# Kernel optimization log

Hardware: AMD Instinct MI355X
Metric: run time of the kernel (lower is better)

## Reference

```python
import jax, jax.numpy as jnp
import numpy as np

NUM_FEATURE = 512
HIDDEN = 256
NUM_CLASSES = 10
L1 = 1e-4
ALPHA = 1e-3
BATCH = 65536


def setup_inputs() -> dict:
    key = jax.random.key(0)
    k = jax.random.split(key, 6)
    x = jax.random.normal(k[0], (BATCH, NUM_FEATURE), dtype=jnp.float32)
    y = jax.random.randint(k[1], (BATCH,), 0, NUM_CLASSES, dtype=jnp.int32)
    fc0 = jax.random.normal(k[2], (NUM_FEATURE, 512), dtype=jnp.float32) / NUM_FEATURE
    fc1 = jax.random.normal(k[3], (NUM_FEATURE, 512), dtype=jnp.float32) / NUM_FEATURE
    w = jax.random.normal(k[4], (NUM_FEATURE, HIDDEN), dtype=jnp.float32) / NUM_FEATURE
    w1 = jax.random.normal(k[5], (HIDDEN, NUM_CLASSES), dtype=jnp.float32) / HIDDEN
    return {"x": x, "y": y, "fc0": fc0, "fc1": fc1, "w": w, "w1": w1}


def reference(x, y, fc0, fc1, w, w1):
    # sigmoid-gated MLP block with residual
    x1 = x @ fc0                                   # [B, 512]
    x2 = jax.nn.relu(x @ fc1)                      # [B, 512]
    x4 = x + (1.0 + jax.nn.sigmoid(x1)) * x2       # [B, 512] residual

    # head (Dropout(p=0.0) is identity)
    logits = jax.nn.relu(x4 @ w) @ w1              # [B, 10]
    pred = jnp.argmax(logits, axis=1)

    # cross-entropy (mean over batch)
    logp = jax.nn.log_softmax(logits, axis=-1)
    ce = -jnp.mean(jnp.take_along_axis(logp, y[:, None].astype(jnp.int32), axis=1))

    # L1 penalty on all weight matrices
    l1_pen = L1 * (jnp.abs(w1).sum() + jnp.abs(w).sum()
                   + jnp.abs(fc0).sum() + jnp.abs(fc1).sum())

    # per-class variance: sum_i ||mean_{y_i} - x4_i||^2, vectorized via segment sums
    counts = jax.ops.segment_sum(jnp.ones((x4.shape[0],), jnp.float32), y,
                                 num_segments=NUM_CLASSES)
    sums = jax.ops.segment_sum(x4, y, num_segments=NUM_CLASSES)   # [10, 512]
    means = sums / jnp.maximum(counts, 1.0)[:, None]
    var_loss = jnp.sum(jnp.square(means[y] - x4))

    loss = ce + l1_pen + ALPHA * var_loss
    acc = jnp.mean((pred.astype(jnp.int32) == y.astype(jnp.int32)).astype(jnp.float32))
    return (loss, acc)
```

## Files before the change

### kernel.cpp

```cpp
#include <hip/hip_runtime.h>
#include <stdint.h>

#define BATCH 65536
#define FDIM 512
#define HDIM 256
#define NC 10
#define NREP 16

typedef short short8 __attribute__((ext_vector_type(8)));
typedef float f32x4 __attribute__((ext_vector_type(4)));

#define OFF_FC0T   ((size_t)0)
#define OFF_FC1T   (OFF_FC0T + (size_t)512*512*2)
#define OFF_WT     (OFF_FC1T + (size_t)512*512*2)
#define OFF_XT     (OFF_WT   + (size_t)256*512*2)
#define OFF_X4T    (OFF_XT   + (size_t)BATCH*512*2)
#define OFF_ACC    (OFF_X4T  + (size_t)BATCH*512*2)
#define SCAL_SUMSQ 0
#define SCAL_CE    16
#define SCAL_ACC   32
#define SCAL_L1    48
#define SCAL_N     128
#define CNT_OFF    SCAL_N
#define GSUM_OFF   (SCAL_N + NREP*16)
#define ACC_FLOATS (GSUM_OFF + NREP*5120)
#define OFF_W1T    (OFF_ACC + (size_t)ACC_FLOATS*4)

#define GLL(g,l) __builtin_amdgcn_global_load_lds((const __attribute__((address_space(1))) void*)(g), (__attribute__((address_space(3))) void*)(l), 16, 0, 0)

__device__ __forceinline__ unsigned short f2b(float f){
  unsigned u = __float_as_uint(f);
  u += 0x7FFFu + ((u >> 16) & 1u);
  return (unsigned short)(u >> 16);
}
__device__ __forceinline__ float b2f(unsigned short h){
  return __uint_as_float(((unsigned)h) << 16);
}
__device__ __forceinline__ unsigned pk2b(float f0, float f1){
  unsigned u0 = __float_as_uint(f0) + 0x8000u;
  unsigned u1 = __float_as_uint(f1) + 0x8000u;
  return __builtin_amdgcn_perm(u1, u0, 0x07060302u);
}

__global__ __launch_bounds__(256) void k_setup(
    const float* __restrict__ x,   const float* __restrict__ fc0,
    const float* __restrict__ fc1, const float* __restrict__ w,
    const float* __restrict__ w1,  const int* __restrict__ y,
    unsigned short* __restrict__ xT,   unsigned short* __restrict__ fc0T,
    unsigned short* __restrict__ fc1T, unsigned short* __restrict__ wT,
    unsigned short* __restrict__ w1T,  float* __restrict__ accb)
{
  int blk = blockIdx.x, t = threadIdx.x;
  if (blk < 1024){
    int I = blk*4 + (t >> 6);
    int l = t & 63;
    int row = I*16 + (l & 15), q = l >> 4;
    const float* src = x + (size_t)row*FDIM + q*8;
    #pragma unroll
    for (int C = 0; C < 16; ++C){
      float4 v0 = *(const float4*)(src + C*32);
      float4 v1 = *(const float4*)(src + C*32 + 4);
      unsigned o[4];
      o[0] = pk2b(v0.x, v0.y); o[1] = pk2b(v0.z, v0.w);
      o[2] = pk2b(v1.x, v1.y); o[3] = pk2b(v1.z, v1.w);
      *(short8*)&xT[(((size_t)I*16 + C) << 9) + l*8] = *(short8*)o;
    }
    return;
  }
  if (blk < 1360){
    int i = (blk - 1024)*256 + t;
    float l1v = 0.f;
    if (i < 32768){
      int n4 = i&15, m = (i>>4)&3, C = (i>>6)&15, J = i>>10;
      int n = J*16+n4, k8 = C*4+m;
      unsigned short o[8];
      #pragma unroll
      for (int j=0;j<8;++j){ float v = fc0[(size_t)(k8*8+j)*512 + n]; o[j]=f2b(v); l1v += fabsf(v); }
      *(short8*)&fc0T[(size_t)(J*16+C)*512 + (i&63)*8] = *(short8*)o;
    } else if (i < 65536){
      int j0 = i - 32768;
      int n4 = j0&15, m = (j0>>4)&3, C = (j0>>6)&15, J = j0>>10;
      int n = J*16+n4, k8 = C*4+m;
      unsigned short o[8];
      #pragma unroll
      for (int j=0;j<8;++j){ float v = fc1[(size_t)(k8*8+j)*512 + n]; o[j]=f2b(v); l1v += fabsf(v); }
      *(short8*)&fc1T[(size_t)(J*16+C)*512 + (j0&63)*8] = *(short8*)o;
    } else if (i < 81920){
      int j0 = i - 65536;
      int n4 = j0&15, m = (j0>>4)&3, C = (j0>>6)&15, J = j0>>10;
      int n = J*16+n4, k8 = C*4+m;
      unsigned short o[8];
      #pragma unroll
      for (int j=0;j<8;++j){ float v = w[(size_t)(k8*8+j)*256 + n]; o[j]=f2b(v); l1v += fabsf(v); }
      *(short8*)&wT[(size_t)(J*16+C)*512 + (j0&63)*8] = *(short8*)o;
    } else if (i < 86016){
      int j0 = i - 81920;
      int C = j0 >> 9, l = (j0 >> 3) & 63, e = j0 & 7;
      int n = l & 15, k = C*32 + (l>>4)*8 + e;
      float v = (n < NC) ? w1[k*NC + n] : 0.f;
      w1T[C*512 + l*8 + e] = f2b(v);
      if (n < NC) l1v = fabsf(v);
    }
    for (int off = 32; off; off >>= 1) l1v += __shfl_down(l1v, off);
    if ((t & 63) == 0 && l1v != 0.f)
      atomicAdd(&accb[SCAL_L1 + (blk & (NREP-1))], l1v);
    return;
  }
  if (blk < 1441){
    int base = (blk - 1360)*1024;
    #pragma unroll
    for (int j=0;j<4;++j){
      int idx = base + j*256 + t;
      if (idx < ACC_FLOATS && (idx < CNT_OFF || idx >= CNT_OFF + NREP*16))
        accb[idx] = 0.f;
    }
    return;
  }
  {
    __shared__ float cntS[16];
    int b = blk - 1441;
    if (t < 16) cntS[t] = 0.f;
    __syncthreads();
    int base = b*4096;
    for (int i = t; i < 4096; i += 256) atomicAdd(&cntS[y[base+i]], 1.f);
    __syncthreads();
    if (t < 16) accb[CNT_OFF + b*16 + t] = cntS[t];
  }
}


#define BARRIER() __builtin_amdgcn_s_barrier()
#define LGKM0() do{ asm volatile("s_waitcnt lgkmcnt(0)" ::: "memory"); \
                    __builtin_amdgcn_sched_barrier(0); }while(0)

#define READA(A, AB, H) do{                                                   \
  _Pragma("unroll") for (int c_=0;c_<2;++c_)                                  \
  _Pragma("unroll") for (int m_=0;m_<4;++m_)                                  \
    A[c_][m_] = *(const short8*)((AB) + (((wr*8 + (H)*4 + m_)*2 + c_)<<10) + lane*16); \
}while(0)

#define READB(B, BB, MAT) do{                                                 \
  _Pragma("unroll") for (int c_=0;c_<2;++c_)                                  \
  _Pragma("unroll") for (int n_=0;n_<2;++n_)                                  \
    B[c_][n_] = *(const short8*)((BB) + (MAT)*16384 + (((wc*2+n_)*2 + c_)<<10) + lane*16); \
}while(0)

#define MMALL(MB) do{                                                         \
  __builtin_amdgcn_s_setprio(1);                                              \
  _Pragma("unroll") for (int c_=0;c_<2;++c_)                                  \
  _Pragma("unroll") for (int n_=0;n_<2;++n_)                                  \
  _Pragma("unroll") for (int m_=0;m_<4;++m_)                                  \
    acc1[(MB)+m_][n_] = __builtin_amdgcn_mfma_f32_16x16x32_bf16(a[c_][m_], b0[c_][n_], acc1[(MB)+m_][n_], 0,0,0); \
  _Pragma("unroll") for (int c_=0;c_<2;++c_)                                  \
  _Pragma("unroll") for (int n_=0;n_<2;++n_)                                  \
  _Pragma("unroll") for (int m_=0;m_<4;++m_)                                  \
    acc2[(MB)+m_][n_] = __builtin_amdgcn_mfma_f32_16x16x32_bf16(a[c_][m_], b1[c_][n_], acc2[(MB)+m_][n_], 0,0,0); \
  __builtin_amdgcn_s_setprio(0);                                              \
}while(0)

#define STAGEA(KT2, H) do{                                                    \
  char* d_ = ldsd + (((KT2)&1) ? 65536 : 0);                                  \
  _Pragma("unroll") for (int r_=0;r_<2;++r_){                                 \
    int idx_ = r_*8 + wv, q_ = idx_>>1, C_ = idx_&1;                          \
    int Il_ = (q_&3) + ((q_>>2)<<3) + (H)*4;                                  \
    GLL(xb + (((size_t)((rowblk*16 + Il_)*16 + (KT2)*2 + C_)) << 10) + lane*16, \
        d_ + ((Il_*2 + C_) << 10) + lane*16);                                 \
  } }while(0)

#define STAGEB(KT2, MAT) do{                                                  \
  char* d_ = ldsd + (((KT2)&1) ? 65536 : 0) + 32768 + (MAT)*16384;            \
  const char* s_ = (MAT) ? b1b : b0b;                                         \
  _Pragma("unroll") for (int r_=0;r_<2;++r_){                                 \
    int idx_ = r_*8 + wv, J_ = idx_>>1, C_ = idx_&1;                          \
    GLL(s_ + (((size_t)((colblk*8 + J_)*16 + (KT2)*2 + C_)) << 10) + lane*16, \
        d_ + ((J_*2 + C_) << 10) + lane*16);                                  \
  } }while(0)

#define KLOOP_PROLOGUE() do{                                                  \
  STAGEA(0,0); STAGEA(0,1); STAGEB(0,0); STAGEB(0,1);                         \
  STAGEA(1,0); STAGEB(1,0);                                                   \
  asm volatile("s_waitcnt vmcnt(4)" ::: "memory");                            \
  __builtin_amdgcn_sched_barrier(0);                                          \
  BARRIER();                                                                  \
}while(0)

#define KLOOP_BODY(kt) do{                                                    \
  char* Ab = ldsd + (((kt)&1) ? 65536 : 0);                                   \
  char* Bb = Ab + 32768;                                                      \
                                                                      \
  READA(a, Ab, 0);                                                            \
  READB(b0, Bb, 0);                                                           \
  READB(b1, Bb, 1);                                                           \
  if ((kt) < 7){ STAGEA((kt)+1, 1); STAGEB((kt)+1, 1); }                      \
  BARRIER(); LGKM0();                                                         \
  MMALL(0);                                                                   \
  BARRIER();                                                                  \
                                                                      \
  READA(a, Ab, 1);                                                            \
  if ((kt) < 6){ STAGEA((kt)+2, 0); STAGEB((kt)+2, 0); }                      \
  BARRIER(); LGKM0();                                                         \
  MMALL(4);                                                                   \
  if ((kt) < 6)       { asm volatile("s_waitcnt vmcnt(4)" ::: "memory"); }    \
  else if ((kt) == 6) { asm volatile("s_waitcnt vmcnt(0)" ::: "memory"); }    \
  __builtin_amdgcn_sched_barrier(0);                                          \
  BARRIER();                                                                  \
}while(0)

__global__ __launch_bounds__(512, 2) void k_gemm12(
    const unsigned short* __restrict__ xT,
    const unsigned short* __restrict__ fc0T,
    const unsigned short* __restrict__ fc1T,
    unsigned short* __restrict__ x4T,
    float* __restrict__ scal)
{
  extern __shared__ __align__(16) char ldsd[];

  int blk = blockIdx.x;
  int wg = (blk & 7)*128 + (blk >> 3);
  int rowblk = wg >> 2;
  int colblk = wg & 3;

  int t = threadIdx.x;
  int wv = t >> 6, lane = t & 63, ln = lane & 15, quad = lane >> 4;
  int wr = wv >> 2, wc = wv & 3;

  const char* xb  = (const char*)xT;
  const char* b0b = (const char*)fc0T;
  const char* b1b = (const char*)fc1T;

  const f32x4 zv = {0.f,0.f,0.f,0.f};
  f32x4 acc1[8][2], acc2[8][2];
  #pragma unroll
  for (int m=0;m<8;++m){ acc1[m][0]=zv; acc1[m][1]=zv; acc2[m][0]=zv; acc2[m][1]=zv; }

  short8 a[2][4], b0[2][2], b1[2][2];

  KLOOP_PROLOGUE();
  for (int kt = 0; kt < 8; ++kt) KLOOP_BODY(kt);

  {
    int Cres = colblk*4 + wc;
    #pragma unroll
    for (int i = 0; i < 8; ++i){
      GLL(xb + (((size_t)((rowblk*16 + wr*8 + i)*16 + Cres)) << 10) + lane*16,
          ldsd + ((wv*8 + i) << 10) + lane*16);
    }
    asm volatile("s_waitcnt vmcnt(0)" ::: "memory");
  }
  __syncthreads();

  unsigned short* resU = (unsigned short*)ldsd;
  unsigned short* x4U  = (unsigned short*)(ldsd + 65536);
  float sumsq = 0.f;
  #pragma unroll
  for (int m = 0; m < 8; ++m){
    #pragma unroll
    for (int n = 0; n < 2; ++n){
      #pragma unroll
      for (int r = 0; r < 4; ++r){
        int slot = (quad*4 + r) | ((n*2 + (ln>>3)) << 4);
        int idx = ((wv*8 + m) << 9) + slot*8 + (ln & 7);
        float xv  = b2f(resU[idx]);
        float x1v = acc1[m][n][r];
        float x2v = fmaxf(acc2[m][n][r], 0.f);
        float gate = 1.f + 1.f/(1.f + __expf(-x1v));
        float x4v = fmaf(gate, x2v, xv);
        unsigned short ub = f2b(x4v);
        float fq = b2f(ub);
        sumsq = fmaf(fq, fq, sumsq);
        x4U[idx] = ub;
      }
    }
  }
  for (int off = 32; off; off >>= 1) sumsq += __shfl_down(sumsq, off);
  __syncthreads();
  float* red = (float*)ldsd;
  if (lane == 0) red[wv] = sumsq;
  __syncthreads();
  if (t == 0){
    float s = 0.f;
    #pragma unroll
    for (int i=0;i<8;++i) s += red[i];
    atomicAdd(&scal[SCAL_SUMSQ + (blk & (NREP-1))], s);
  }
  #pragma unroll
  for (int r = 0; r < 2; ++r){
    int o = r*512 + t;
    int tile = o >> 6, off16 = o & 63;
    int wvp = tile >> 3, i = tile & 7;
    size_t Ig = (size_t)rowblk*16 + (wvp>>2)*8 + i;
    int Cg = colblk*4 + (wvp & 3);
    *(short8*)&x4T[((Ig*16 + Cg) << 9) + off16*8] =
      *(const short8*)&x4U[(tile << 9) + off16*8];
  }
}

__global__ __launch_bounds__(256) void k_csum(const unsigned short* __restrict__ x4T,
                                              const int* __restrict__ y,
                                              float* __restrict__ gsum){
  int w = blockIdx.x*4 + (threadIdx.x >> 6);
  int l = threadIdx.x & 63;
  int C = w & 15, Ig = w >> 4;
  int rl = l & 15, q = l >> 4;
  float a[NC][8];
  #pragma unroll
  for (int c=0;c<NC;++c)
    #pragma unroll
    for (int e=0;e<8;++e) a[c][e]=0.f;
  for (int ii = 0; ii < 64; ++ii){
    int I = Ig*64 + ii;
    int yv = y[I*16 + rl];
    short8 v = *(const short8*)&x4T[(((size_t)I*16 + C) << 9) + l*8];
    float f[8];
    #pragma unroll
    for (int e=0;e<8;++e) f[e] = b2f((unsigned short)v[e]);
    #pragma unroll
    for (int c=0;c<NC;++c){
      bool m = (yv == c);
      #pragma unroll
      for (int e=0;e<8;++e) a[c][e] += m ? f[e] : 0.f;
    }
  }
  #pragma unroll
  for (int off = 1; off < 16; off <<= 1)
    #pragma unroll
    for (int c=0;c<NC;++c)
      #pragma unroll
      for (int e=0;e<8;++e) a[c][e] += __shfl_xor(a[c][e], off);
  if (rl == 0){
    int rep = Ig & (NREP-1);
    int kb = C*32 + q*8;
    #pragma unroll
    for (int c=0;c<NC;++c)
      #pragma unroll
      for (int e=0;e<8;++e)
        atomicAdd(&gsum[(size_t)rep*5120 + c*512 + kb + e], a[c][e]);
  }
}

__global__ __launch_bounds__(512, 2) void k_gemm3_head(
    const unsigned short* __restrict__ x4T,
    const unsigned short* __restrict__ wT,
    const unsigned short* __restrict__ w1T,
    const int* __restrict__ y,
    float* __restrict__ scal)
{
  extern __shared__ __align__(16) char ldsd[];
  __shared__ float redc[8], reda[8];

  int blk = blockIdx.x;
  int rowblk = blk;
  const int colblk = 0;

  int t = threadIdx.x;
  int wv = t >> 6, lane = t & 63, ln = lane & 15, quad = lane >> 4;
  int wr = wv >> 2, wc = wv & 3;
  int rep = (blk ^ (blk >> 4)) & (NREP-1);

  const char* xb  = (const char*)x4T;
  const char* b0b = (const char*)wT;
  const char* b1b = (const char*)wT + (size_t)128*1024;

  const f32x4 zv = {0.f,0.f,0.f,0.f};
  f32x4 acc1[8][2], acc2[8][2];
  #pragma unroll
  for (int m=0;m<8;++m){ acc1[m][0]=zv; acc1[m][1]=zv; acc2[m][0]=zv; acc2[m][1]=zv; }

  short8 a[2][4], b0[2][2], b1[2][2];

  KLOOP_PROLOGUE();
  for (int kt = 0; kt < 8; ++kt) KLOOP_BODY(kt);

  short8 bw1[8];
  #pragma unroll
  for (int Ck = 0; Ck < 8; ++Ck)
    bw1[Ck] = *(const short8*)&w1T[Ck*512 + lane*8];

  unsigned short* transH = (unsigned short*)ldsd;
  #pragma unroll
  for (int m = 0; m < 8; ++m){
    #pragma unroll
    for (int n = 0; n < 2; ++n){
      #pragma unroll
      for (int r = 0; r < 4; ++r){
        int slot = (quad*4 + r) | ((n*2 + (ln>>3)) << 4);
        int e = ln & 7;
        int IhA = wr*8 + m;
        transH[((IhA*8 + wc)     << 9) + slot*8 + e] = f2b(fmaxf(acc1[m][n][r], 0.f));
        transH[((IhA*8 + 4 + wc) << 9) + slot*8 + e] = f2b(fmaxf(acc2[m][n][r], 0.f));
      }
    }
  }
  __syncthreads();

  f32x4 alog[2] = {zv, zv};
  #pragma unroll
  for (int ih = 0; ih < 2; ++ih){
    int Ih = wv*2 + ih;
    #pragma unroll
    for (int Ck = 0; Ck < 8; ++Ck){
      short8 af = *(const short8*)&transH[((Ih*8 + Ck) << 9) + lane*8];
      alog[ih] = __builtin_amdgcn_mfma_f32_16x16x32_bf16(af, bw1[Ck], alog[ih], 0,0,0);
    }
  }

  float ce_l = 0.f, acc_l = 0.f;
  #pragma unroll
  for (int ih = 0; ih < 2; ++ih){
    #pragma unroll
    for (int r = 0; r < 4; ++r){
      int grow = blk*256 + (wv*2 + ih)*16 + quad*4 + r;
      int yv = y[grow];
      float lg = (ln < NC) ? alog[ih][r] : -1e30f;
      float m = lg; int mi = ln;
      #pragma unroll
      for (int mk = 1; mk < 16; mk <<= 1){
        float om = __shfl_xor(m, mk); int oi = __shfl_xor(mi, mk);
        if (om > m || (om == m && oi < mi)){ m = om; mi = oi; }
      }
      float e  = (ln < NC) ? __expf(lg - m) : 0.f;
      float sy = (ln == yv) ? lg : 0.f;
      #pragma unroll
      for (int mk = 1; mk < 16; mk <<= 1){ e += __shfl_xor(e, mk); sy += __shfl_xor(sy, mk); }
      float lse = m + __logf(e);
      if (ln == 0){ ce_l += (lse - sy); acc_l += (mi == yv) ? 1.f : 0.f; }
    }
  }
  ce_l  += __shfl_down(ce_l, 16);  acc_l += __shfl_down(acc_l, 16);
  ce_l  += __shfl_down(ce_l, 32);  acc_l += __shfl_down(acc_l, 32);
  if (lane == 0){ redc[wv] = ce_l; reda[wv] = acc_l; }
  __syncthreads();
  if (t == 0){
    float c = 0.f, aa = 0.f;
    #pragma unroll
    for (int i=0;i<8;++i){ c += redc[i]; aa += reda[i]; }
    atomicAdd(&scal[SCAL_CE  + rep], c);
    atomicAdd(&scal[SCAL_ACC + rep], aa);
  }
}

__global__ __launch_bounds__(1024) void k_final(const float* __restrict__ accb,
                                                float* __restrict__ out){
  const float* gsum = accb + GSUM_OFF;
  const float* gcnt = accb + CNT_OFF;
  int t = threadIdx.x;
  float contrib = 0.f;
  for (int idx = t; idx < 5120; idx += 1024){
    float S = 0.f;
    #pragma unroll
    for (int r = 0; r < NREP; ++r) S += gsum[(size_t)r*5120 + idx];
    int c = idx >> 9;
    float cnt = 0.f;
    #pragma unroll
    for (int r = 0; r < NREP; ++r) cnt += gcnt[r*16 + c];
    contrib += S*S / fmaxf(cnt, 1.f);
  }
  for (int off = 32; off; off >>= 1) contrib += __shfl_down(contrib, off);
  __shared__ float red[16];
  if ((t & 63) == 0) red[t >> 6] = contrib;
  __syncthreads();
  if (t == 0){
    float var2 = 0.f;
    #pragma unroll
    for (int i=0;i<16;++i) var2 += red[i];
    float sumsq=0.f, ce=0.f, acc=0.f, l1=0.f;
    for (int r=0;r<NREP;++r){
      sumsq += accb[SCAL_SUMSQ+r];
      ce    += accb[SCAL_CE+r];
      acc   += accb[SCAL_ACC+r];
      l1    += accb[SCAL_L1+r];
    }
    float var_loss = sumsq - var2;
    out[0] = ce/(float)BATCH + 1e-4f*l1 + 1e-3f*var_loss;
    out[1] = acc/(float)BATCH;
  }
}

extern "C" void kernel_launch(void* const* d_in, const int* in_sizes, int n_in,
                              void* d_out, int out_size, void* d_ws, size_t ws_size,
                              hipStream_t stream){
  (void)in_sizes; (void)n_in; (void)out_size; (void)ws_size;
  const float* x   = (const float*)d_in[0];
  const int*   y   = (const int*)d_in[1];
  const float* fc0 = (const float*)d_in[2];
  const float* fc1 = (const float*)d_in[3];
  const float* w   = (const float*)d_in[4];
  const float* w1  = (const float*)d_in[5];
  char* ws = (char*)d_ws;
  unsigned short* fc0T = (unsigned short*)(ws + OFF_FC0T);
  unsigned short* fc1T = (unsigned short*)(ws + OFF_FC1T);
  unsigned short* wT   = (unsigned short*)(ws + OFF_WT);
  unsigned short* xT   = (unsigned short*)(ws + OFF_XT);
  unsigned short* x4T  = (unsigned short*)(ws + OFF_X4T);
  unsigned short* w1T  = (unsigned short*)(ws + OFF_W1T);
  float* accb = (float*)(ws + OFF_ACC);
  float* scal = accb;
  float* gsum = accb + GSUM_OFF;

  static bool once = [](){
    hipFuncSetAttribute((const void*)k_gemm12,
                        hipFuncAttributeMaxDynamicSharedMemorySize, 131072);
    hipFuncSetAttribute((const void*)k_gemm3_head,
                        hipFuncAttributeMaxDynamicSharedMemorySize, 131072);
    return true;
  }();
  (void)once;

  k_setup<<<1457, 256, 0, stream>>>(x, fc0, fc1, w, w1, y, xT, fc0T, fc1T, wT, w1T, accb);
  k_gemm12<<<1024, 512, 131072, stream>>>(xT, fc0T, fc1T, x4T, scal);
  k_csum<<<256, 256, 0, stream>>>(x4T, y, gsum);
  k_gemm3_head<<<256, 512, 131072, stream>>>(x4T, wT, w1T, y, scal);
  k_final<<<1, 1024, 0, stream>>>(accb, (float*)d_out);
}
```

Baseline: 399.3 us.

## Restructure GEMM k-loop into finer stages with per-K-chunk register fragments

Replaces the two-phase k-loop body with an eight-phase schedule per pair of k-tiles. Each phase loads one K-chunk of A (all 8 row fragments) and a single B fragment pair, then runs 16 MFMAs on acc1 or acc2. Global-to-LDS staging is split into smaller per-chunk pieces interleaved across the phases. The aim is to cut register pressure for the A/B fragments and spread memory traffic more evenly against MFMA work. The cost is more barriers and waits per k-tile, plus reloading A fragments for each chunk.

```diff
diff --git a/kernel.cpp b/kernel.cpp
--- a/kernel.cpp
+++ b/kernel.cpp
@@ -133,77 +133,98 @@
 #define LGKM0() do{ asm volatile("s_waitcnt lgkmcnt(0)" ::: "memory"); \
                     __builtin_amdgcn_sched_barrier(0); }while(0)
 
-#define READA(A, AB, H) do{                                                   \
-  _Pragma("unroll") for (int c_=0;c_<2;++c_)                                  \
-  _Pragma("unroll") for (int m_=0;m_<4;++m_)                                  \
-    A[c_][m_] = *(const short8*)((AB) + (((wr*8 + (H)*4 + m_)*2 + c_)<<10) + lane*16); \
+#define RA(AB, C) do{                                                         \
+  _Pragma("unroll") for (int m_=0;m_<8;++m_)                                  \
+    a[m_] = *(const short8*)((AB) + (((wr*8+m_)*2 + (C))<<10) + lane*16);     \
 }while(0)
 
-#define READB(B, BB, MAT) do{                                                 \
-  _Pragma("unroll") for (int c_=0;c_<2;++c_)                                  \
+#define RB(AB, MAT, C) do{                                                    \
   _Pragma("unroll") for (int n_=0;n_<2;++n_)                                  \
-    B[c_][n_] = *(const short8*)((BB) + (MAT)*16384 + (((wc*2+n_)*2 + c_)<<10) + lane*16); \
+    bb[n_] = *(const short8*)((AB) + 32768 + (MAT)*16384 +                    \
+                              (((wc*2+n_)*2 + (C))<<10) + lane*16);           \
 }while(0)
 
-#define MMALL(MB) do{                                                         \
+#define MM16(ACC) do{                                                         \
   __builtin_amdgcn_s_setprio(1);                                              \
-  _Pragma("unroll") for (int c_=0;c_<2;++c_)                                  \
   _Pragma("unroll") for (int n_=0;n_<2;++n_)                                  \
-  _Pragma("unroll") for (int m_=0;m_<4;++m_)                                  \
-    acc1[(MB)+m_][n_] = __builtin_amdgcn_mfma_f32_16x16x32_bf16(a[c_][m_], b0[c_][n_], acc1[(MB)+m_][n_], 0,0,0); \
-  _Pragma("unroll") for (int c_=0;c_<2;++c_)                                  \
-  _Pragma("unroll") for (int n_=0;n_<2;++n_)                                  \
-  _Pragma("unroll") for (int m_=0;m_<4;++m_)                                  \
-    acc2[(MB)+m_][n_] = __builtin_amdgcn_mfma_f32_16x16x32_bf16(a[c_][m_], b1[c_][n_], acc2[(MB)+m_][n_], 0,0,0); \
+  _Pragma("unroll") for (int m_=0;m_<8;++m_)                                  \
+    ACC[m_][n_] = __builtin_amdgcn_mfma_f32_16x16x32_bf16(a[m_], bb[n_], ACC[m_][n_], 0,0,0); \
   __builtin_amdgcn_s_setprio(0);                                              \
 }while(0)
 
-#define STAGEA(KT2, H) do{                                                    \
-  char* d_ = ldsd + (((KT2)&1) ? 65536 : 0);                                  \
+#define SA(KT, C) do{                                                         \
+  char* d_ = ldsd + (((KT)&1) ? 65536 : 0);                                   \
   _Pragma("unroll") for (int r_=0;r_<2;++r_){                                 \
-    int idx_ = r_*8 + wv, q_ = idx_>>1, C_ = idx_&1;                          \
-    int Il_ = (q_&3) + ((q_>>2)<<3) + (H)*4;                                  \
-    GLL(xb + (((size_t)((rowblk*16 + Il_)*16 + (KT2)*2 + C_)) << 10) + lane*16, \
-        d_ + ((Il_*2 + C_) << 10) + lane*16);                                 \
+    int I_ = wv + r_*8;                                                       \
+    GLL(xb + (((size_t)((rowblk*16 + I_)*16 + (KT)*2 + (C))) << 10) + lane*16,\
+        d_ + ((I_*2 + (C)) << 10) + lane*16);                                 \
   } }while(0)
 
-#define STAGEB(KT2, MAT) do{                                                  \
-  char* d_ = ldsd + (((KT2)&1) ? 65536 : 0) + 32768 + (MAT)*16384;            \
-  const char* s_ = (MAT) ? b1b : b0b;                                         \
-  _Pragma("unroll") for (int r_=0;r_<2;++r_){                                 \
-    int idx_ = r_*8 + wv, J_ = idx_>>1, C_ = idx_&1;                          \
-    GLL(s_ + (((size_t)((colblk*8 + J_)*16 + (KT2)*2 + C_)) << 10) + lane*16, \
-        d_ + ((J_*2 + C_) << 10) + lane*16);                                  \
-  } }while(0)
-
-#define KLOOP_PROLOGUE() do{                                                  \
-  STAGEA(0,0); STAGEA(0,1); STAGEB(0,0); STAGEB(0,1);                         \
-  STAGEA(1,0); STAGEB(1,0);                                                   \
-  asm volatile("s_waitcnt vmcnt(4)" ::: "memory");                            \
+#define SB(KT, C) do{                                                         \
+  char* d_ = ldsd + (((KT)&1) ? 65536 : 0) + 32768;                           \
+  GLL(b0b + (((size_t)((colblk*8 + wv)*16 + (KT)*2 + (C))) << 10) + lane*16,  \
+      d_ + ((wv*2 + (C)) << 10) + lane*16);                                   \
+  GLL(b1b + (((size_t)((colblk*8 + wv)*16 + (KT)*2 + (C))) << 10) + lane*16,  \
+      d_ + 16384 + ((wv*2 + (C)) << 10) + lane*16);                           \
+}while(0)
+
+#define KLOOP() do{                                                           \
+             \
+  SA(0,0); SB(0,0); SA(0,1); SB(0,1); SA(1,0); SB(1,0); SA(1,1);              \
+  asm volatile("s_waitcnt vmcnt(6)" ::: "memory");                            \
   __builtin_amdgcn_sched_barrier(0);                                          \
   BARRIER();                                                                  \
-}while(0)
-
-#define KLOOP_BODY(kt) do{                                                    \
-  char* Ab = ldsd + (((kt)&1) ? 65536 : 0);                                   \
-  char* Bb = Ab + 32768;                                                      \
-                                                                      \
-  READA(a, Ab, 0);                                                            \
-  READB(b0, Bb, 0);                                                           \
-  READB(b1, Bb, 1);                                                           \
-  if ((kt) < 7){ STAGEA((kt)+1, 1); STAGEB((kt)+1, 1); }                      \
-  BARRIER(); LGKM0();                                                         \
-  MMALL(0);                                                                   \
-  BARRIER();                                                                  \
-                                                                      \
-  READA(a, Ab, 1);                                                            \
-  if ((kt) < 6){ STAGEA((kt)+2, 0); STAGEB((kt)+2, 0); }                      \
-  BARRIER(); LGKM0();                                                         \
-  MMALL(4);                                                                   \
-  if ((kt) < 6)       { asm volatile("s_waitcnt vmcnt(4)" ::: "memory"); }    \
-  else if ((kt) == 6) { asm volatile("s_waitcnt vmcnt(0)" ::: "memory"); }    \
-  __builtin_amdgcn_sched_barrier(0);                                          \
-  BARRIER();                                                                  \
+  _Pragma("unroll")                                                           \
+  for (int i = 0; i < 4; ++i){                                                \
+    int kt0 = 2*i, kt1 = 2*i+1;                                               \
+    char* Ab0 = ldsd + ((kt0 & 1) ? 65536 : 0);                               \
+    char* Ab1 = ldsd + ((kt1 & 1) ? 65536 : 0);                               \
+                                                                     \
+    RA(Ab0, 0); RB(Ab0, 0, 0);                                                \
+    SB(kt1, 1);                                                               \
+    BARRIER(); LGKM0(); MM16(acc1);                                           \
+    BARRIER();                                                                \
+                                                                     \
+    RB(Ab0, 1, 0);                                                            \
+    if (i < 3) SA(kt0+2, 0);                                                  \
+    BARRIER(); LGKM0(); MM16(acc2);                                           \
+    BARRIER();                                                                \
+                                                                     \
+    RA(Ab0, 1); RB(Ab0, 0, 1);                                                \
+    if (i < 3) SB(kt0+2, 0);                                                  \
+    BARRIER(); LGKM0(); MM16(acc1);                                           \
+    BARRIER();                                                                \
+                                                                     \
+    RB(Ab0, 1, 1);                                                            \
+    if (i < 3) SA(kt0+2, 1);                                                  \
+    BARRIER(); LGKM0(); MM16(acc2);                                           \
+    if (i < 3) { asm volatile("s_waitcnt vmcnt(6)" ::: "memory"); }           \
+    else       { asm volatile("s_waitcnt vmcnt(0)" ::: "memory"); }           \
+    __builtin_amdgcn_sched_barrier(0);                                        \
+    BARRIER();                                                                \
+                                                                     \
+    RA(Ab1, 0); RB(Ab1, 0, 0);                                                \
+    if (i < 3) SB(kt0+2, 1);                                                  \
+    BARRIER(); LGKM0(); MM16(acc1);                                           \
+    BARRIER();                                                                \
+                                                                     \
+    RB(Ab1, 1, 0);                                                            \
+    if (i < 3) SA(kt1+2, 0);                                                  \
+    BARRIER(); LGKM0(); MM16(acc2);                                           \
+    BARRIER();                                                                \
+                                                                     \
+    RA(Ab1, 1); RB(Ab1, 0, 1);                                                \
+    if (i < 3) SB(kt1+2, 0);                                                  \
+    BARRIER(); LGKM0(); MM16(acc1);                                           \
+    BARRIER();                                                                \
+                                                                     \
+    RB(Ab1, 1, 1);                                                            \
+    if (i < 3) SA(kt1+2, 1);                                                  \
+    BARRIER(); LGKM0(); MM16(acc2);                                           \
+    if (i < 3) { asm volatile("s_waitcnt vmcnt(6)" ::: "memory");             \
+                 __builtin_amdgcn_sched_barrier(0); }                         \
+    BARRIER();                                                                \
+  }                                                                           \
 }while(0)
 
 __global__ __launch_bounds__(512, 2) void k_gemm12(
@@ -233,10 +254,9 @@
   #pragma unroll
   for (int m=0;m<8;++m){ acc1[m][0]=zv; acc1[m][1]=zv; acc2[m][0]=zv; acc2[m][1]=zv; }
 
-  short8 a[2][4], b0[2][2], b1[2][2];
-
-  KLOOP_PROLOGUE();
-  for (int kt = 0; kt < 8; ++kt) KLOOP_BODY(kt);
+  short8 a[8], bb[2];
+
+  KLOOP();
 
   {
     int Cres = colblk*4 + wc;
@@ -366,10 +386,9 @@
   #pragma unroll
   for (int m=0;m<8;++m){ acc1[m][0]=zv; acc1[m][1]=zv; acc2[m][0]=zv; acc2[m][1]=zv; }
 
-  short8 a[2][4], b0[2][2], b1[2][2];
-
-  KLOOP_PROLOGUE();
-  for (int kt = 0; kt < 8; ++kt) KLOOP_BODY(kt);
+  short8 a[8], bb[2];
+
+  KLOOP();
 
   short8 bw1[8];
   #pragma unroll
```

Result: no change. 401.2 us (+0.5%).
